# Performance work log

Measured on AMD Instinct MI355X. Metric: run time of the kernel, lower is better.

Reference implementation:

```python
import jax, jax.numpy as jnp
import numpy as np

HIDDEN = 2048
NUM_HEADS = 16
NUM_KV_HEADS = 4
HEAD_DIM = HIDDEN // NUM_HEADS  # 128
GROUP = NUM_HEADS // NUM_KV_HEADS  # 4
SCALE = HEAD_DIM ** -0.5


def setup_inputs() -> dict:
    key = jax.random.key(0)
    ks = jax.random.split(key, 9)
    B, S = 2, 2048
    kv_dim = HEAD_DIM * NUM_KV_HEADS
    std = HIDDEN ** -0.5
    return {
        "x": jax.random.normal(ks[0], (B, S, HIDDEN), dtype=jnp.float32),
        "Wq": jax.random.normal(ks[1], (HIDDEN, HIDDEN), dtype=jnp.float32) * std,
        "bq": jnp.zeros((HIDDEN,), dtype=jnp.float32),
        "Wk": jax.random.normal(ks[2], (HIDDEN, kv_dim), dtype=jnp.float32) * std,
        "bk": jnp.zeros((kv_dim,), dtype=jnp.float32),
        "Wv": jax.random.normal(ks[3], (HIDDEN, kv_dim), dtype=jnp.float32) * std,
        "bv": jnp.zeros((kv_dim,), dtype=jnp.float32),
        "Wo": jax.random.normal(ks[4], (HIDDEN, HIDDEN), dtype=jnp.float32) * std,
        "bo": jnp.zeros((HIDDEN,), dtype=jnp.float32),
    }


def reference(x, Wq, bq, Wk, bk, Wv, bv, Wo, bo):
    B, S, _ = x.shape
    # projections
    q = (x @ Wq + bq).reshape(B, S, NUM_KV_HEADS, GROUP, HEAD_DIM)  # grouped query heads
    k = (x @ Wk + bk).reshape(B, S, NUM_KV_HEADS, HEAD_DIM)
    v = (x @ Wv + bv).reshape(B, S, NUM_KV_HEADS, HEAD_DIM)
    # scores: [B, Hkv, G, Sq, Sk] -- same math as repeat_interleave of K/V over G,
    # but K/V are broadcast over the group axis instead of materialized.
    attn = jnp.einsum("bqhgd,bkhd->bhgqk", q, k) * SCALE
    attn = jax.nn.softmax(attn, axis=-1)
    out = jnp.einsum("bhgqk,bkhd->bqhgd", attn, v).reshape(B, S, HIDDEN)
    return out @ Wo + bo
```

## Files before the change

kernel.cpp:

```cpp
#include <hip/hip_runtime.h>


#define SEQ    2048
#define HIDDEN 2048

typedef __attribute__((ext_vector_type(8))) short v8s;
typedef __attribute__((ext_vector_type(4))) float v4f;

#define MFMA16(a,b,c) __builtin_amdgcn_mfma_f32_16x16x32_bf16((a),(b),(c),0,0,0)

__device__ __forceinline__ ushort f2b(float f){
  unsigned u = __float_as_uint(f);
  u += 0x7fffu + ((u >> 16) & 1u);
  return (ushort)(u >> 16);
}

__device__ __forceinline__ void gload16(const void* g, void* l){
  __builtin_amdgcn_global_load_lds((const __attribute__((address_space(1))) void*)g,
                                   (__attribute__((address_space(3))) void*)l, 16, 0, 0);
}

#define WAIT_VM0   0x0F70
#define WAIT_LGKM0 0xC07F

__global__ void k_conv(const float* __restrict__ in, ushort* __restrict__ out, int n){
  int i = (blockIdx.x*256 + threadIdx.x)*4;
  if (i >= n) return;
  float4 f = *(const float4*)(in + i);
  ushort4 u; u.x=f2b(f.x); u.y=f2b(f.y); u.z=f2b(f.z); u.w=f2b(f.w);
  *(ushort4*)(out + i) = u;
}

__global__ void k_tconv(const float* __restrict__ in, ushort* __restrict__ out,
                        int rows, int cols){
  __shared__ float t[32][33];
  int tx = threadIdx.x & 31, ty = threadIdx.x >> 5;
  int c0 = blockIdx.x*32, r0 = blockIdx.y*32;
#pragma unroll
  for (int i=0;i<4;i++) t[ty+i*8][tx] = in[(size_t)(r0+ty+i*8)*cols + c0+tx];
  __syncthreads();
#pragma unroll
  for (int i=0;i<4;i++) out[(size_t)(c0+ty+i*8)*rows + r0+tx] = f2b(t[tx][ty+i*8]);
}

__global__ void k_tv(const ushort* __restrict__ vb, ushort* __restrict__ vT){
  __shared__ ushort t[32][33];
  int tx = threadIdx.x & 31, ty = threadIdx.x >> 5;
  int s0 = blockIdx.x*32, d0 = blockIdx.y*32, bh = blockIdx.z;
  int b = bh >> 2, h = bh & 3;
  const ushort* src = vb + (size_t)b*SEQ*512 + h*128;
#pragma unroll
  for (int i=0;i<4;i++) t[ty+i*8][tx] = src[(size_t)(s0+ty+i*8)*512 + d0+tx];
  __syncthreads();
  ushort* dst = vT + (size_t)bh*128*SEQ;
#pragma unroll
  for (int i=0;i<4;i++) dst[(size_t)(d0+ty+i*8)*SEQ + s0+tx] = t[tx][ty+i*8];
}

#define GEMM_MAIN(A_, Bt_, K_)                                                        \
  __shared__ ushort sA[128*32], sB[128*32];                                           \
  const int tid = threadIdx.x, lane = tid & 63, wid = tid >> 6;                       \
  const int wm = wid >> 1, wn = wid & 1, lm = lane & 15, q8 = (lane >> 4)*8;          \
  const int rowB = blockIdx.y*128, colB = blockIdx.x*128;                             \
  v4f acc[4][4] = {};                                                                 \
  for (int k0 = 0; k0 < (K_); k0 += 32){                                              \
    _Pragma("unroll")                                                                 \
    for (int it=0; it<2; it++){                                                       \
      int c = tid + it*256;                                                           \
      gload16((A_)  + (size_t)(rowB + (c>>2))*(K_) + k0 + (c&3)*8, (char*)sA + c*16); \
      gload16((Bt_) + (size_t)(colB + (c>>2))*(K_) + k0 + (c&3)*8, (char*)sB + c*16); \
    }                                                                                 \
    __syncthreads();                                                                  \
    v8s af[4], bfr[4];                                                                \
    _Pragma("unroll")                                                                 \
    for (int i=0;i<4;i++){                                                            \
      af[i]  = *(const v8s*)(sA + (wm*64 + i*16 + lm)*32 + q8);                       \
      bfr[i] = *(const v8s*)(sB + (wn*64 + i*16 + lm)*32 + q8);                       \
    }                                                                                 \
    _Pragma("unroll")                                                                 \
    for (int i=0;i<4;i++)                                                             \
      _Pragma("unroll")                                                               \
      for (int j=0;j<4;j++) acc[i][j] = MFMA16(af[i], bfr[j], acc[i][j]);             \
    __syncthreads();                                                                  \
  }                                                                                   \
  const int quad = lane >> 4;

__global__ __launch_bounds__(256) void k_gemm_qkv(
    const ushort* __restrict__ A, const ushort* __restrict__ Bt,
    const float* __restrict__ bq, const float* __restrict__ bk, const float* __restrict__ bv,
    ushort* __restrict__ qb, ushort* __restrict__ kb, ushort* __restrict__ vb){
  GEMM_MAIN(A, Bt, HIDDEN)
#pragma unroll
  for (int i=0;i<4;i++)
#pragma unroll
  for (int j=0;j<4;j++){
    int col = colB + wn*64 + j*16 + lm;
#pragma unroll
    for (int r=0;r<4;r++){
      int row = rowB + wm*64 + i*16 + quad*4 + r;
      float v = acc[i][j][r];
      if (col < 2048)      qb[(size_t)row*2048 + col]        = f2b(v + bq[col]);
      else if (col < 2560) kb[(size_t)row*512 + (col-2048)]  = f2b(v + bk[col-2048]);
      else                 vb[(size_t)row*512 + (col-2560)]  = f2b(v + bv[col-2560]);
    }
  }
}

__global__ __launch_bounds__(256) void k_gemm_out(
    const ushort* __restrict__ A, const ushort* __restrict__ Bt,
    const float* __restrict__ bo, float* __restrict__ out){
  GEMM_MAIN(A, Bt, HIDDEN)
#pragma unroll
  for (int i=0;i<4;i++)
#pragma unroll
  for (int j=0;j<4;j++){
    int col = colB + wn*64 + j*16 + lm;
#pragma unroll
    for (int r=0;r<4;r++){
      int row = rowB + wm*64 + i*16 + quad*4 + r;
      out[(size_t)row*2048 + col] = acc[i][j][r] + bo[col];
    }
  }
}

__global__ __launch_bounds__(256, 1) void k_attn(
    const ushort* __restrict__ qb, const ushort* __restrict__ kb,
    const ushort* __restrict__ vT, ushort* __restrict__ Ob){
  __shared__ ushort sK[2][64*128];
  __shared__ ushort sV[2][128*64];
  __shared__ ushort sP[4][4096];
  const int tid = threadIdx.x, lane = tid & 63, w = tid >> 6;
  const int lm = lane & 15, quad = lane >> 4, q8 = quad*8;
  const int pair = blockIdx.x & 7;
  const int hkv = pair & 3, b = pair >> 2;
  const int qt = (blockIdx.x >> 3) & 7, g = blockIdx.x >> 6;
  const int head = hkv*4 + g;
  const float C = 0.08838834764831845f * 1.4426950408889634f;

  const ushort* kbb = kb + (size_t)b*SEQ*512 + hkv*128;
  const ushort* vbb = vT + (size_t)(b*4+hkv)*128*SEQ;

  const int kk = lane >> 4, ksw = lane & 15;
  const int dd = lane >> 3, vsw = lane & 7;

#define STAGE_K(t, buf) { _Pragma("unroll") for (int i=0;i<4;i++){                     \
    int c = w*4 + i; int key = c*4 + kk; int wd = ksw ^ (key & 15);                    \
    gload16(kbb + (size_t)((t)*64 + key)*512 + wd*8, &sK[buf][c*512 + lane*8]); } }
#define STAGE_V(t, buf) { _Pragma("unroll") for (int i=0;i<4;i++){                     \
    int c = w*4 + i; int drow = c*8 + dd; int wd = vsw ^ dd;                           \
    gload16(vbb + (size_t)drow*SEQ + (t)*64 + wd*8, &sV[buf][c*512 + lane*8]); } }

  v8s qf[4][4];
#pragma unroll
  for (int rb=0; rb<4; rb++)
#pragma unroll
    for (int ks=0; ks<4; ks++)
      qf[rb][ks] = *(const v8s*)(qb + (size_t)(b*SEQ + qt*256 + w*64 + rb*16 + lm)*HIDDEN
                                    + head*128 + ks*32 + q8);

  v4f o[4][8] = {};
  float lreg[4] = {0.f, 0.f, 0.f, 0.f};

  STAGE_K(0, 0)
  STAGE_V(0, 0)
  __builtin_amdgcn_s_waitcnt(WAIT_VM0);
  __syncthreads();

  for (int t=0; t<32; t++){
    const int cur = t & 1;
    if (t < 31) STAGE_K(t+1, cur^1)

    v8s kf[4][4];
#pragma unroll
    for (int kt=0; kt<4; kt++)
#pragma unroll
      for (int ks=0; ks<4; ks++)
        kf[kt][ks] = *(const v8s*)(&sK[cur][(kt*16+lm)*128 + ((ks*4+quad)^lm)*8]);

    v4f sacc[4][4] = {};
#pragma unroll
    for (int ks=0; ks<4; ks++)
#pragma unroll
      for (int kt=0; kt<4; kt++)
#pragma unroll
        for (int rb=0; rb<4; rb++)
          sacc[rb][kt] = MFMA16(kf[kt][ks], qf[rb][ks], sacc[rb][kt]);

#pragma unroll
    for (int rb=0; rb<4; rb++){
      float rs = 0.f;
#pragma unroll
      for (int kt=0; kt<4; kt++){
        float p0 = __builtin_amdgcn_exp2f(sacc[rb][kt][0]*C);
        float p1 = __builtin_amdgcn_exp2f(sacc[rb][kt][1]*C);
        float p2 = __builtin_amdgcn_exp2f(sacc[rb][kt][2]*C);
        float p3 = __builtin_amdgcn_exp2f(sacc[rb][kt][3]*C);
        rs += (p0+p1)+(p2+p3);
        uint2 pk;
        pk.x = (unsigned)f2b(p0) | ((unsigned)f2b(p1) << 16);
        pk.y = (unsigned)f2b(p2) | ((unsigned)f2b(p3) << 16);
        int kc = kt >> 1;
        int dl = ((kt&1)*2 + (quad>>1))*16 + lm;
        *(uint2*)(&sP[w][(rb*2+kc)*512 + dl*8 + (quad&1)*4]) = pk;
      }
      lreg[rb] += rs;
    }

    __builtin_amdgcn_s_waitcnt(WAIT_VM0);
    __syncthreads();
    if (t < 31) STAGE_V(t+1, cur^1)

    __builtin_amdgcn_s_waitcnt(WAIT_LGKM0);
    v8s pa[4][2];
#pragma unroll
    for (int rb=0; rb<4; rb++)
#pragma unroll
      for (int kc=0; kc<2; kc++)
        pa[rb][kc] = *(const v8s*)(&sP[w][(rb*2+kc)*512 + lane*8]);
    v8s vf[8][2];
#pragma unroll
    for (int dt=0; dt<8; dt++)
#pragma unroll
      for (int kc=0; kc<2; kc++)
        vf[dt][kc] = *(const v8s*)(&sV[cur][(dt*16+lm)*64 + ((kc*4+quad)^(lm&7))*8]);
#pragma unroll
    for (int kc=0; kc<2; kc++)
#pragma unroll
      for (int dt=0; dt<8; dt++)
#pragma unroll
        for (int rb=0; rb<4; rb++)
          o[rb][dt] = MFMA16(pa[rb][kc], vf[dt][kc], o[rb][dt]);
  }

#pragma unroll
  for (int rb=0; rb<4; rb++){
    float lv = lreg[rb];
    lv += __shfl_xor(lv, 16);
    lv += __shfl_xor(lv, 32);
    float inv[4];
#pragma unroll
    for (int r=0;r<4;r++) inv[r] = 1.0f / __shfl(lv, (lane & 48) + quad*4 + r);
#pragma unroll
    for (int dt=0; dt<8; dt++)
#pragma unroll
      for (int r=0;r<4;r++){
        int row = b*SEQ + qt*256 + w*64 + rb*16 + quad*4 + r;
        int col = head*128 + dt*16 + lm;
        Ob[(size_t)row*HIDDEN + col] = f2b(o[rb][dt][r]*inv[r]);
      }
  }
#undef STAGE_K
#undef STAGE_V
}

extern "C" void kernel_launch(void* const* d_in, const int* in_sizes, int n_in,
                              void* d_out, int out_size, void* d_ws, size_t ws_size,
                              hipStream_t stream){
  const float* x  = (const float*)d_in[0];
  const float* Wq = (const float*)d_in[1];
  const float* bq = (const float*)d_in[2];
  const float* Wk = (const float*)d_in[3];
  const float* bk = (const float*)d_in[4];
  const float* Wv = (const float*)d_in[5];
  const float* bv = (const float*)d_in[6];
  const float* Wo = (const float*)d_in[7];
  const float* bo = (const float*)d_in[8];
  float* out = (float*)d_out;

  ushort* xb  = (ushort*)d_ws;
  ushort* Wt  = xb  + 8388608;
  ushort* Wto = Wt  + 6291456;
  ushort* qb  = Wto + 4194304;
  ushort* kb  = qb  + 8388608;
  ushort* vb  = kb  + 2097152;
  ushort* vT  = vb  + 2097152;
  ushort* Ob  = vT  + 2097152;

  k_conv <<<8192, 256, 0, stream>>>(x, xb, 8388608);
  k_tconv<<<dim3(64,64), 256, 0, stream>>>(Wq, Wt, 2048, 2048);
  k_tconv<<<dim3(16,64), 256, 0, stream>>>(Wk, Wt + 4194304, 2048, 512);
  k_tconv<<<dim3(16,64), 256, 0, stream>>>(Wv, Wt + 5242880, 2048, 512);
  k_tconv<<<dim3(64,64), 256, 0, stream>>>(Wo, Wto, 2048, 2048);
  k_gemm_qkv<<<dim3(24,32), 256, 0, stream>>>(xb, Wt, bq, bk, bv, qb, kb, vb);
  k_tv  <<<dim3(64,4,8), 256, 0, stream>>>(vb, vT);
  k_attn<<<256, 256, 0, stream>>>(qb, kb, vT, Ob);
  k_gemm_out<<<dim3(16,32), 256, 0, stream>>>(Ob, Wto, bo, out);
}
```

Measured before the change: 351.6 us.

## Halve attention block size, move P through lane shuffles instead of LDS

The attention kernel now uses 128-thread blocks (2 waves) covering 128 query rows, launched as 512 blocks instead of 256. This gives more blocks to spread across CUs. The softmax probabilities no longer take a round trip through shared memory: each wave rebuilds the MFMA A-operand with cross-lane shuffles, so the sP buffer and one barrier and LDS wait are gone. K and V for the next tile are now prefetched together at the top of the loop. The cost is that each K/V tile loaded to LDS is reused by fewer query rows, which doubles total K/V traffic, and the shuffles add extra ALU work.

```diff
diff --git a/kernel.cpp b/kernel.cpp
--- a/kernel.cpp
+++ b/kernel.cpp
@@ -21,7 +21,6 @@
 }
 
 #define WAIT_VM0   0x0F70
-#define WAIT_LGKM0 0xC07F
 
 __global__ void k_conv(const float* __restrict__ in, ushort* __restrict__ out, int n){
   int i = (blockIdx.x*256 + threadIdx.x)*4;
@@ -123,17 +122,16 @@
   }
 }
 
-__global__ __launch_bounds__(256, 1) void k_attn(
+__global__ __launch_bounds__(128, 1) void k_attn(
     const ushort* __restrict__ qb, const ushort* __restrict__ kb,
     const ushort* __restrict__ vT, ushort* __restrict__ Ob){
   __shared__ ushort sK[2][64*128];
   __shared__ ushort sV[2][128*64];
-  __shared__ ushort sP[4][4096];
   const int tid = threadIdx.x, lane = tid & 63, w = tid >> 6;
   const int lm = lane & 15, quad = lane >> 4, q8 = quad*8;
   const int pair = blockIdx.x & 7;
   const int hkv = pair & 3, b = pair >> 2;
-  const int qt = (blockIdx.x >> 3) & 7, g = blockIdx.x >> 6;
+  const int qt = (blockIdx.x >> 3) & 15, g = blockIdx.x >> 7;
   const int head = hkv*4 + g;
   const float C = 0.08838834764831845f * 1.4426950408889634f;
 
@@ -143,11 +141,11 @@
   const int kk = lane >> 4, ksw = lane & 15;
   const int dd = lane >> 3, vsw = lane & 7;
 
-#define STAGE_K(t, buf) { _Pragma("unroll") for (int i=0;i<4;i++){                     \
-    int c = w*4 + i; int key = c*4 + kk; int wd = ksw ^ (key & 15);                    \
+#define STAGE_K(t, buf) { _Pragma("unroll") for (int i=0;i<8;i++){                     \
+    int c = w*8 + i; int key = c*4 + kk; int wd = ksw ^ (key & 15);                    \
     gload16(kbb + (size_t)((t)*64 + key)*512 + wd*8, &sK[buf][c*512 + lane*8]); } }
-#define STAGE_V(t, buf) { _Pragma("unroll") for (int i=0;i<4;i++){                     \
-    int c = w*4 + i; int drow = c*8 + dd; int wd = vsw ^ dd;                           \
+#define STAGE_V(t, buf) { _Pragma("unroll") for (int i=0;i<8;i++){                     \
+    int c = w*8 + i; int drow = c*8 + dd; int wd = vsw ^ dd;                           \
     gload16(vbb + (size_t)drow*SEQ + (t)*64 + wd*8, &sV[buf][c*512 + lane*8]); } }
 
   v8s qf[4][4];
@@ -155,7 +153,7 @@
   for (int rb=0; rb<4; rb++)
 #pragma unroll
     for (int ks=0; ks<4; ks++)
-      qf[rb][ks] = *(const v8s*)(qb + (size_t)(b*SEQ + qt*256 + w*64 + rb*16 + lm)*HIDDEN
+      qf[rb][ks] = *(const v8s*)(qb + (size_t)(b*SEQ + qt*128 + w*64 + rb*16 + lm)*HIDDEN
                                     + head*128 + ks*32 + q8);
 
   v4f o[4][8] = {};
@@ -168,24 +166,23 @@
 
   for (int t=0; t<32; t++){
     const int cur = t & 1;
-    if (t < 31) STAGE_K(t+1, cur^1)
-
-    v8s kf[4][4];
-#pragma unroll
-    for (int kt=0; kt<4; kt++)
+    if (t < 31){ STAGE_K(t+1, cur^1) STAGE_V(t+1, cur^1) }
+
+    v4f sacc[4][4] = {};
+#pragma unroll
+    for (int kt=0; kt<4; kt++){
+      v8s kf[4];
 #pragma unroll
       for (int ks=0; ks<4; ks++)
-        kf[kt][ks] = *(const v8s*)(&sK[cur][(kt*16+lm)*128 + ((ks*4+quad)^lm)*8]);
-
-    v4f sacc[4][4] = {};
-#pragma unroll
-    for (int ks=0; ks<4; ks++)
-#pragma unroll
-      for (int kt=0; kt<4; kt++)
+        kf[ks] = *(const v8s*)(&sK[cur][(kt*16+lm)*128 + ((ks*4+quad)^lm)*8]);
+#pragma unroll
+      for (int ks=0; ks<4; ks++)
 #pragma unroll
         for (int rb=0; rb<4; rb++)
-          sacc[rb][kt] = MFMA16(kf[kt][ks], qf[rb][ks], sacc[rb][kt]);
-
+          sacc[rb][kt] = MFMA16(kf[ks], qf[rb][ks], sacc[rb][kt]);
+    }
+
+    uint2 pk[4][4];
 #pragma unroll
     for (int rb=0; rb<4; rb++){
       float rs = 0.f;
@@ -196,40 +193,48 @@
         float p2 = __builtin_amdgcn_exp2f(sacc[rb][kt][2]*C);
         float p3 = __builtin_amdgcn_exp2f(sacc[rb][kt][3]*C);
         rs += (p0+p1)+(p2+p3);
-        uint2 pk;
-        pk.x = (unsigned)f2b(p0) | ((unsigned)f2b(p1) << 16);
-        pk.y = (unsigned)f2b(p2) | ((unsigned)f2b(p3) << 16);
-        int kc = kt >> 1;
-        int dl = ((kt&1)*2 + (quad>>1))*16 + lm;
-        *(uint2*)(&sP[w][(rb*2+kc)*512 + dl*8 + (quad&1)*4]) = pk;
+        pk[rb][kt].x = (unsigned)f2b(p0) | ((unsigned)f2b(p1) << 16);
+        pk[rb][kt].y = (unsigned)f2b(p2) | ((unsigned)f2b(p3) << 16);
       }
       lreg[rb] += rs;
     }
 
+    const int slo = ((quad & 1) << 5) + lm;
+    const bool hi = (quad >> 1) != 0;
+    v8s pa[4][2];
+#pragma unroll
+    for (int rb=0; rb<4; rb++)
+#pragma unroll
+      for (int kc=0; kc<2; kc++){
+        union { uint u[4]; v8s s; } pu;
+        unsigned ax = __shfl((int)pk[rb][2*kc].x,   slo);
+        unsigned ay = __shfl((int)pk[rb][2*kc].y,   slo);
+        unsigned bx = __shfl((int)pk[rb][2*kc+1].x, slo);
+        unsigned by = __shfl((int)pk[rb][2*kc+1].y, slo);
+        unsigned cx = __shfl((int)pk[rb][2*kc].x,   slo+16);
+        unsigned cy = __shfl((int)pk[rb][2*kc].y,   slo+16);
+        unsigned dx = __shfl((int)pk[rb][2*kc+1].x, slo+16);
+        unsigned dy = __shfl((int)pk[rb][2*kc+1].y, slo+16);
+        pu.u[0] = hi ? bx : ax;  pu.u[1] = hi ? by : ay;
+        pu.u[2] = hi ? dx : cx;  pu.u[3] = hi ? dy : cy;
+        pa[rb][kc] = pu.s;
+      }
+
+#pragma unroll
+    for (int dt=0; dt<8; dt++){
+      v8s vf[2];
+#pragma unroll
+      for (int kc=0; kc<2; kc++)
+        vf[kc] = *(const v8s*)(&sV[cur][(dt*16+lm)*64 + ((kc*4+quad)^(lm&7))*8]);
+#pragma unroll
+      for (int kc=0; kc<2; kc++)
+#pragma unroll
+        for (int rb=0; rb<4; rb++)
+          o[rb][dt] = MFMA16(pa[rb][kc], vf[kc], o[rb][dt]);
+    }
+
     __builtin_amdgcn_s_waitcnt(WAIT_VM0);
     __syncthreads();
-    if (t < 31) STAGE_V(t+1, cur^1)
-
-    __builtin_amdgcn_s_waitcnt(WAIT_LGKM0);
-    v8s pa[4][2];
-#pragma unroll
-    for (int rb=0; rb<4; rb++)
-#pragma unroll
-      for (int kc=0; kc<2; kc++)
-        pa[rb][kc] = *(const v8s*)(&sP[w][(rb*2+kc)*512 + lane*8]);
-    v8s vf[8][2];
-#pragma unroll
-    for (int dt=0; dt<8; dt++)
-#pragma unroll
-      for (int kc=0; kc<2; kc++)
-        vf[dt][kc] = *(const v8s*)(&sV[cur][(dt*16+lm)*64 + ((kc*4+quad)^(lm&7))*8]);
-#pragma unroll
-    for (int kc=0; kc<2; kc++)
-#pragma unroll
-      for (int dt=0; dt<8; dt++)
-#pragma unroll
-        for (int rb=0; rb<4; rb++)
-          o[rb][dt] = MFMA16(pa[rb][kc], vf[dt][kc], o[rb][dt]);
   }
 
 #pragma unroll
@@ -244,7 +249,7 @@
     for (int dt=0; dt<8; dt++)
 #pragma unroll
       for (int r=0;r<4;r++){
-        int row = b*SEQ + qt*256 + w*64 + rb*16 + quad*4 + r;
+        int row = b*SEQ + qt*128 + w*64 + rb*16 + quad*4 + r;
         int col = head*128 + dt*16 + lm;
         Ob[(size_t)row*HIDDEN + col] = f2b(o[rb][dt][r]*inv[r]);
       }
@@ -283,6 +288,6 @@
   k_tconv<<<dim3(64,64), 256, 0, stream>>>(Wo, Wto, 2048, 2048);
   k_gemm_qkv<<<dim3(24,32), 256, 0, stream>>>(xb, Wt, bq, bk, bv, qb, kb, vb);
   k_tv  <<<dim3(64,4,8), 256, 0, stream>>>(vb, vT);
-  k_attn<<<256, 256, 0, stream>>>(qb, kb, vT, Ob);
+  k_attn<<<512, 128, 0, stream>>>(qb, kb, vT, Ob);
   k_gemm_out<<<dim3(16,32), 256, 0, stream>>>(Ob, Wto, bo, out);
 }
```

Measured after the change: 366.8 us. 1.04x slower.
